# Kernel optimization log

Hardware: AMD Instinct MI355X
Metric: run time of the kernel (lower is better)

The kernel has to match this reference:

```python
import jax, jax.numpy as jnp
import numpy as np

# RT-DETR multi-scale deformable attention reference (PPMSDeformableAttention forward, value_mask=None)
SPATIAL_SHAPES = ((80, 80), (40, 40), (20, 20))  # (H, W) per level; sum(H*W) = 8400 = Len_v
NUM_HEADS = 8
NUM_LEVELS = 3
NUM_POINTS = 4


def _gather_corner(v_l, ix, iy, H, W):
    # v_l: [bs, heads, H*W, hd]; ix/iy: [bs, heads, N] int32 pixel indices (possibly out of range)
    valid = (ix >= 0) & (ix < W) & (iy >= 0) & (iy < H)
    idx = jnp.clip(iy, 0, H - 1) * W + jnp.clip(ix, 0, W - 1)
    g = jnp.take_along_axis(v_l, idx[..., None], axis=2)  # [bs, heads, N, hd]
    return jnp.where(valid[..., None], g, jnp.zeros((), v_l.dtype))


def _bilinear_sample(v_l, px, py, H, W):
    # grid_sample(align_corners=False, padding_mode='zeros') semantics.
    # v_l: [bs, heads, H*W, hd]; px/py: [bs, heads, N] continuous pixel coords
    x0 = jnp.floor(px).astype(jnp.int32)
    y0 = jnp.floor(py).astype(jnp.int32)
    x1, y1 = x0 + 1, y0 + 1
    wx1 = px - x0.astype(px.dtype)
    wy1 = py - y0.astype(py.dtype)
    wx0, wy0 = 1.0 - wx1, 1.0 - wy1
    out = (_gather_corner(v_l, x0, y0, H, W) * (wx0 * wy0)[..., None]
           + _gather_corner(v_l, x1, y0, H, W) * (wx1 * wy0)[..., None]
           + _gather_corner(v_l, x0, y1, H, W) * (wx0 * wy1)[..., None]
           + _gather_corner(v_l, x1, y1, H, W) * (wx1 * wy1)[..., None])
    return out  # [bs, heads, N, hd]


def setup_inputs() -> dict:
    key = jax.random.key(0)
    ks = jax.random.split(key, 8)
    bs, Lq, C = 32, 300, 256
    Lv = sum(h * w for h, w in SPATIAL_SHAPES)
    tp = NUM_HEADS * NUM_LEVELS * NUM_POINTS  # 96
    s = 1.0 / np.sqrt(C)
    return {
        "query": jax.random.normal(ks[0], (bs, Lq, C), jnp.float32),
        "reference_points": jax.random.uniform(ks[1], (bs, Lq, NUM_LEVELS, 4), jnp.float32, 0.05, 0.95),
        "value": jax.random.normal(ks[2], (bs, Lv, C), jnp.float32),
        "Wv": jax.random.normal(ks[3], (C, C), jnp.float32) * s,
        "bv": jnp.zeros((C,), jnp.float32),
        "Woff": jax.random.normal(ks[4], (C, tp * 2), jnp.float32) * (s * 0.1),
        "boff": jax.random.normal(ks[5], (tp * 2,), jnp.float32) * 0.5,
        "Watt": jax.random.normal(ks[6], (C, tp), jnp.float32) * s,
        "batt": jnp.zeros((tp,), jnp.float32),
        "Wout": jax.random.normal(ks[7], (C, C), jnp.float32) * s,
        "bout": jnp.zeros((C,), jnp.float32),
    }


def reference(query, reference_points, value, Wv, bv, Woff, boff, Watt, batt, Wout, bout):
    bs, Lq, C = query.shape
    H_, L, P = NUM_HEADS, NUM_LEVELS, NUM_POINTS
    hd = C // H_
    Lv = value.shape[1]

    # value projection -> [bs, heads, Lv, hd]
    v = (value @ Wv + bv).reshape(bs, Lv, H_, hd).transpose(0, 2, 1, 3)

    # sampling offsets and attention weights from query
    off = (query @ Woff + boff).reshape(bs, Lq, H_, L, P, 2)
    attw = jax.nn.softmax((query @ Watt + batt).reshape(bs, Lq, H_, L * P), axis=-1)
    attw = attw.reshape(bs, Lq, H_, L, P)

    # reference_points last dim == 4: (cx, cy, w, h) normalized
    ref_xy = reference_points[:, :, None, :, None, :2]  # [bs,Lq,1,L,1,2]
    ref_wh = reference_points[:, :, None, :, None, 2:]
    loc = ref_xy + off / P * ref_wh * 0.5  # [bs,Lq,H,L,P,2], normalized [0,1]

    out = jnp.zeros((bs, Lq, H_, hd), query.dtype)
    start = 0
    for l, (H, W) in enumerate(SPATIAL_SHAPES):
        v_l = v[:, :, start:start + H * W]  # [bs, heads, H*W, hd]
        start += H * W
        # normalized -> pixel coords (align_corners=False): p = loc * size - 0.5
        locl = loc[:, :, :, l]  # [bs, Lq, heads, P, 2]
        px = locl[..., 0] * W - 0.5
        py = locl[..., 1] * H - 0.5
        # [bs, Lq, heads, P] -> [bs, heads, Lq*P]
        px = px.transpose(0, 2, 1, 3).reshape(bs, H_, Lq * P)
        py = py.transpose(0, 2, 1, 3).reshape(bs, H_, Lq * P)
        sampled = _bilinear_sample(v_l, px, py, H, W)  # [bs, heads, Lq*P, hd]
        sampled = sampled.reshape(bs, H_, Lq, P, hd)
        out = out + jnp.einsum('bhqpd,bqhp->bqhd', sampled, attw[:, :, :, l])

    out = out.reshape(bs, Lq, C)
    return out @ Wout + bout
```

## Files before the change

kernel.cpp:

```cpp
#include <hip/hip_runtime.h>
#include <hip/hip_bf16.h>

#define BS 32
#define LQ 300
#define CDIM 256
#define HEADS 8
#define HD 32
#define NLEVELS 3
#define NPOINTS 4
#define LV 8400
#define NOA 288

typedef __attribute__((ext_vector_type(4))) float f32x4;
typedef __attribute__((ext_vector_type(8))) short short8;
typedef __attribute__((ext_vector_type(8))) unsigned short u16x8;
typedef __attribute__((ext_vector_type(4))) unsigned short u16x4;

__device__ __forceinline__ unsigned short f2bf(float f) {
    __hip_bfloat16 h = __float2bfloat16(f);
    return __bfloat16_as_ushort(h);
}
__device__ __forceinline__ float bf2f(unsigned short u) {
    union { unsigned u; float f; } v; v.u = ((unsigned)u) << 16;
    return v.f;
}

__global__ void prep_weights_kernel(
    const float* __restrict__ Wv, const float* __restrict__ Wout,
    const float* __restrict__ Woff, const float* __restrict__ Watt,
    unsigned short* __restrict__ WvT, unsigned short* __restrict__ WoutT,
    unsigned short* __restrict__ WoaT)
{
    const int bid = blockIdx.x;
    const int k = threadIdx.x;
    if (bid < 256) {
        WvT[bid * 256 + k] = f2bf(Wv[k * 256 + bid]);
    } else if (bid < 512) {
        const int n = bid - 256;
        WoutT[n * 256 + k] = f2bf(Wout[k * 256 + n]);
    } else {
        const int n = bid - 512;
        const float w = (n < 192) ? Woff[k * 192 + n] : Watt[k * 96 + (n - 192)];
        WoaT[n * 256 + k] = f2bf(w);
    }
}

#define BM 128
#define BMP 64
#define BK 32
#define PAD 40
#define EPAD 264
#define NT (CDIM / BK)

__global__ __launch_bounds__(256) void proj_value_mfma(
    const float* __restrict__ value, const unsigned short* __restrict__ WvT,
    const float* __restrict__ bv, unsigned short* __restrict__ vout)
{
    __shared__ alignas(16) unsigned short lds_w[2][256 * PAD];
    __shared__ alignas(16) unsigned short lds_x[2][BMP * PAD];
    unsigned short* lds_ep = &lds_w[0][0];

    const int tid = threadIdx.x;
    const int lane = tid & 63;
    const int wave = tid >> 6;
    const long row0 = (long)blockIdx.x * BMP;
    const int la = lane & 15;
    const int lg = lane >> 4;

    const unsigned short* wptr = WvT + (size_t)tid * CDIM;
    const int xr = tid >> 2, xk = (tid & 3) * 8;
    const float* xptr = value + (row0 + xr) * CDIM + xk;

    u16x8 wrg[4];
    f32x4 xrg[2];

    auto load_tile = [&](int kb) {
        const u16x8* qw = (const u16x8*)(wptr + kb);
        wrg[0] = qw[0]; wrg[1] = qw[1]; wrg[2] = qw[2]; wrg[3] = qw[3];
        const float* p = xptr + kb;
        xrg[0] = *(const f32x4*)(p);
        xrg[1] = *(const f32x4*)(p + 4);
    };
    auto write_tile = [&](int buf) {
        u16x8* ww = (u16x8*)&lds_w[buf][tid * PAD];
        ww[0] = wrg[0]; ww[1] = wrg[1]; ww[2] = wrg[2]; ww[3] = wrg[3];
        u16x8 t0;
#pragma unroll
        for (int i = 0; i < 4; ++i) {
            t0[i]     = f2bf(xrg[0][i]);
            t0[i + 4] = f2bf(xrg[1][i]);
        }
        *(u16x8*)&lds_x[buf][xr * PAD + xk] = t0;
    };

    f32x4 acc[4][4] = {};

    load_tile(0);
    write_tile(0);
    __syncthreads();
    int cur = 0;

    for (int t = 0; t < NT; ++t) {
        if (t + 1 < NT) load_tile((t + 1) * BK);

        const unsigned short* pw = &lds_w[cur][(wave * 64 + la) * PAD + lg * 8];
        const unsigned short* px = &lds_x[cur][la * PAD + lg * 8];
        short8 xf[4];
#pragma unroll
        for (int mf = 0; mf < 4; ++mf)
            xf[mf] = *(const short8*)(px + mf * 16 * PAD);
#pragma unroll
        for (int nf = 0; nf < 4; ++nf) {
            const short8 wf = *(const short8*)(pw + nf * 16 * PAD);
#pragma unroll
            for (int mf = 0; mf < 4; ++mf)
                acc[nf][mf] = __builtin_amdgcn_mfma_f32_16x16x32_bf16(wf, xf[mf], acc[nf][mf], 0, 0, 0);
        }

        if (t + 1 < NT) write_tile(cur ^ 1);
        __syncthreads();
        cur ^= 1;
    }

#pragma unroll
    for (int nf = 0; nf < 4; ++nf) {
        const int nbase = wave * 64 + nf * 16 + lg * 4;
        const f32x4 bb = *(const f32x4*)&bv[nbase];
#pragma unroll
        for (int mf = 0; mf < 4; ++mf) {
            const int mloc = mf * 16 + la;
            u16x4 o;
#pragma unroll
            for (int j = 0; j < 4; ++j) o[j] = f2bf(acc[nf][mf][j] + bb[j]);
            *(u16x4*)&lds_ep[mloc * EPAD + nbase] = o;
        }
    }
    __syncthreads();
    const int er = tid >> 2;
    const int ec = (tid & 3) * 64;
    const long gr = row0 + er;
    const u16x8* src = (const u16x8*)&lds_ep[er * EPAD + ec];
    u16x8* dst = (u16x8*)&vout[gr * CDIM + ec];
#pragma unroll
    for (int i = 0; i < 8; ++i) dst[i] = src[i];
}

#define APAD 40
#define BPAD 40

__global__ __launch_bounds__(256) void offatt_gemm_mfma(
    const float* __restrict__ query, const unsigned short* __restrict__ WoaT,
    const float* __restrict__ boff, const float* __restrict__ batt,
    float* __restrict__ offatt)
{
    __shared__ unsigned short lds_a[2][BM * APAD];
    __shared__ unsigned short lds_b[2][NOA * BPAD];

    const int tid = threadIdx.x;
    const int lane = tid & 63;
    const int wave = tid >> 6;
    const int wm = wave >> 1;
    const int wn = wave & 1;
    const long row0 = (long)blockIdx.x * BM;

    const int ar = tid >> 1;
    const int ak = (tid & 1) * 16;
    const float* aptr = query + (row0 + ar) * CDIM + ak;
    const unsigned short* bptr  = WoaT + (size_t)tid * CDIM;
    const unsigned short* bptr2 = WoaT + (size_t)(256 + tid) * CDIM;
    const bool extra = tid < 32;

    f32x4 arg[4];
    u16x8 brg[4], brg2[4];

    auto load_tile = [&](int kb) {
        const float* p = aptr + kb;
        arg[0] = *(const f32x4*)(p);
        arg[1] = *(const f32x4*)(p + 4);
        arg[2] = *(const f32x4*)(p + 8);
        arg[3] = *(const f32x4*)(p + 12);
        const u16x8* q = (const u16x8*)(bptr + kb);
        brg[0] = q[0]; brg[1] = q[1]; brg[2] = q[2]; brg[3] = q[3];
        if (extra) {
            const u16x8* q2 = (const u16x8*)(bptr2 + kb);
            brg2[0] = q2[0]; brg2[1] = q2[1]; brg2[2] = q2[2]; brg2[3] = q2[3];
        }
    };
    auto write_tile = [&](int buf) {
        u16x8 t0, t1;
#pragma unroll
        for (int i = 0; i < 4; ++i) {
            t0[i]     = f2bf(arg[0][i]);
            t0[i + 4] = f2bf(arg[1][i]);
            t1[i]     = f2bf(arg[2][i]);
            t1[i + 4] = f2bf(arg[3][i]);
        }
        u16x8* wa = (u16x8*)&lds_a[buf][ar * APAD + ak];
        wa[0] = t0; wa[1] = t1;
        u16x8* wb = (u16x8*)&lds_b[buf][tid * BPAD];
        wb[0] = brg[0]; wb[1] = brg[1]; wb[2] = brg[2]; wb[3] = brg[3];
        if (extra) {
            u16x8* wb2 = (u16x8*)&lds_b[buf][(256 + tid) * BPAD];
            wb2[0] = brg2[0]; wb2[1] = brg2[1]; wb2[2] = brg2[2]; wb2[3] = brg2[3];
        }
    };

    f32x4 acc[4][9] = {};
    const int la = lane & 15;
    const int lg = lane >> 4;

    load_tile(0);
    write_tile(0);
    __syncthreads();
    int cur = 0;

    for (int t = 0; t < CDIM / BK; ++t) {
        if (t + 1 < CDIM / BK) load_tile((t + 1) * BK);

        const unsigned short* pa = &lds_a[cur][(wm * 64 + la) * APAD + lg * 8];
        const unsigned short* pb = &lds_b[cur][(wn * 144 + la) * BPAD + lg * 8];
        short8 af[4];
#pragma unroll
        for (int mi = 0; mi < 4; ++mi)
            af[mi] = *(const short8*)(pa + mi * 16 * APAD);
#pragma unroll
        for (int ni = 0; ni < 9; ++ni) {
            const short8 bf = *(const short8*)(pb + ni * 16 * BPAD);
#pragma unroll
            for (int mi = 0; mi < 4; ++mi)
                acc[mi][ni] = __builtin_amdgcn_mfma_f32_16x16x32_bf16(af[mi], bf, acc[mi][ni], 0, 0, 0);
        }

        if (t + 1 < CDIM / BK) write_tile(cur ^ 1);
        __syncthreads();
        cur ^= 1;
    }

    float bias[9];
#pragma unroll
    for (int ni = 0; ni < 9; ++ni) {
        const int col = wn * 144 + ni * 16 + la;
        bias[ni] = (col < 192) ? boff[col] : batt[col - 192];
    }
#pragma unroll
    for (int mi = 0; mi < 4; ++mi) {
#pragma unroll
        for (int ni = 0; ni < 9; ++ni) {
            const int col = wn * 144 + ni * 16 + la;
#pragma unroll
            for (int j = 0; j < 4; ++j) {
                const long r = row0 + wm * 64 + mi * 16 + lg * 4 + j;
                offatt[r * NOA + col] = acc[mi][ni][j] + bias[ni];
            }
        }
    }
}

__global__ __launch_bounds__(256) void sample_kernel(
    const float* __restrict__ offatt, const float* __restrict__ refpts,
    const unsigned short* __restrict__ v, unsigned short* __restrict__ mid)
{
    __shared__ float oa_s[NOA];
    __shared__ float aw_s[96];
    __shared__ float px_s[96];
    __shared__ float py_s[96];

    const int tid = threadIdx.x;
    const int nb = blockIdx.x;
    const int x = nb & 7;
    const int rest = nb >> 3;
    const int g = rest / LQ;
    const int q = rest % LQ;
    const int b = g * 8 + x;
    const long bq = (long)b * LQ + q;

    oa_s[tid] = offatt[bq * NOA + tid];
    if (tid < 32) oa_s[256 + tid] = offatt[bq * NOA + 256 + tid];
    __syncthreads();

    if (tid < 8) {
        float m = -1e30f;
#pragma unroll
        for (int i = 0; i < 12; ++i) m = fmaxf(m, oa_s[192 + tid * 12 + i]);
        float e[12];
        float s = 0.f;
#pragma unroll
        for (int i = 0; i < 12; ++i) { e[i] = __expf(oa_s[192 + tid * 12 + i] - m); s += e[i]; }
        const float inv = 1.f / s;
#pragma unroll
        for (int i = 0; i < 12; ++i) aw_s[tid * 12 + i] = e[i] * inv;
    }
    if (tid >= 128 && tid < 224) {
        const int t = tid - 128;
        const int h = t / 12, idx = t % 12, l = idx >> 2, p = idx & 3;
        const float* rp = refpts + (bq * NLEVELS + l) * 4;
        const float rx = rp[0], ry = rp[1], rw = rp[2], rh = rp[3];
        const float ox = oa_s[((h * NLEVELS + l) * NPOINTS + p) * 2 + 0];
        const float oy = oa_s[((h * NLEVELS + l) * NPOINTS + p) * 2 + 1];
        const float lx = rx + ox * 0.125f * rw;
        const float ly = ry + oy * 0.125f * rh;
        const int Wl = 80 >> l;
        px_s[t] = lx * (float)Wl - 0.5f;
        py_s[t] = ly * (float)Wl - 0.5f;
    }
    __syncthreads();

    const int h = tid >> 5;
    const int pg = (tid >> 3) & 3;
    const int d4 = tid & 7;
    const unsigned short* vb = v + ((size_t)b * LV) * CDIM + h * HD + d4 * 4;

    float a0 = 0.f, a1 = 0.f, a2 = 0.f, a3 = 0.f;
#pragma unroll
    for (int j = 0; j < 3; ++j) {
        const int i = pg * 3 + j;
        const int l = i >> 2;
        const int idx = h * 12 + i;
        const float px = px_s[idx], py = py_s[idx], aw = aw_s[idx];
        const int Wl = 80 >> l;
        const int start = (l == 0) ? 0 : (l == 1) ? 6400 : 8000;

        const float fx = floorf(px), fy = floorf(py);
        const int x0 = (int)fx, y0 = (int)fy;
        const float wx1 = px - fx, wy1 = py - fy;
        const float wx0 = 1.f - wx1, wy0 = 1.f - wy1;
        const float w00 = wx0 * wy0 * aw, w10 = wx1 * wy0 * aw;
        const float w01 = wx0 * wy1 * aw, w11 = wx1 * wy1 * aw;
        const bool x0v = (unsigned)x0 < (unsigned)Wl;
        const bool x1v = (unsigned)(x0 + 1) < (unsigned)Wl;
        const bool y0v = (unsigned)y0 < (unsigned)Wl;
        const bool y1v = (unsigned)(y0 + 1) < (unsigned)Wl;

        const unsigned short* base = vb + (size_t)start * CDIM;
        if (y0v) {
            const unsigned short* r0p = base + (size_t)(y0 * Wl) * CDIM;
            if (x0v) {
                const u16x4 u = *(const u16x4*)(r0p + (size_t)x0 * CDIM);
                a0 = fmaf(w00, bf2f(u[0]), a0); a1 = fmaf(w00, bf2f(u[1]), a1);
                a2 = fmaf(w00, bf2f(u[2]), a2); a3 = fmaf(w00, bf2f(u[3]), a3);
            }
            if (x1v) {
                const u16x4 u = *(const u16x4*)(r0p + (size_t)(x0 + 1) * CDIM);
                a0 = fmaf(w10, bf2f(u[0]), a0); a1 = fmaf(w10, bf2f(u[1]), a1);
                a2 = fmaf(w10, bf2f(u[2]), a2); a3 = fmaf(w10, bf2f(u[3]), a3);
            }
        }
        if (y1v) {
            const unsigned short* r1p = base + (size_t)((y0 + 1) * Wl) * CDIM;
            if (x0v) {
                const u16x4 u = *(const u16x4*)(r1p + (size_t)x0 * CDIM);
                a0 = fmaf(w01, bf2f(u[0]), a0); a1 = fmaf(w01, bf2f(u[1]), a1);
                a2 = fmaf(w01, bf2f(u[2]), a2); a3 = fmaf(w01, bf2f(u[3]), a3);
            }
            if (x1v) {
                const u16x4 u = *(const u16x4*)(r1p + (size_t)(x0 + 1) * CDIM);
                a0 = fmaf(w11, bf2f(u[0]), a0); a1 = fmaf(w11, bf2f(u[1]), a1);
                a2 = fmaf(w11, bf2f(u[2]), a2); a3 = fmaf(w11, bf2f(u[3]), a3);
            }
        }
    }

    a0 += __shfl_xor(a0, 8);  a1 += __shfl_xor(a1, 8);
    a2 += __shfl_xor(a2, 8);  a3 += __shfl_xor(a3, 8);
    a0 += __shfl_xor(a0, 16); a1 += __shfl_xor(a1, 16);
    a2 += __shfl_xor(a2, 16); a3 += __shfl_xor(a3, 16);

    if (pg == 0) {
        u16x4 o;
        o[0] = f2bf(a0); o[1] = f2bf(a1); o[2] = f2bf(a2); o[3] = f2bf(a3);
        *(u16x4*)&mid[bq * CDIM + h * HD + d4 * 4] = o;
    }
}

__global__ __launch_bounds__(256) void out_gemm_mfma(
    const unsigned short* __restrict__ mid, const unsigned short* __restrict__ WoutT,
    const float* __restrict__ bout, float* __restrict__ out)
{
    __shared__ unsigned short lds_w[2][256 * APAD];
    __shared__ unsigned short lds_x[2][BM * BPAD];

    const int tid = threadIdx.x;
    const int lane = tid & 63;
    const int wave = tid >> 6;
    const int wn = wave & 1;
    const int wm = wave >> 1;
    const long row0 = (long)blockIdx.x * BM;

    const unsigned short* wptr = WoutT + (size_t)tid * CDIM;
    const int xr = tid >> 1;
    const int xk = (tid & 1) * 16;
    const unsigned short* xptr = mid + (row0 + xr) * CDIM + xk;

    u16x8 wrg[4];
    u16x8 xrg[2];

    auto load_tile = [&](int kb) {
        const u16x8* qw = (const u16x8*)(wptr + kb);
        wrg[0] = qw[0]; wrg[1] = qw[1]; wrg[2] = qw[2]; wrg[3] = qw[3];
        const u16x8* qx = (const u16x8*)(xptr + kb);
        xrg[0] = qx[0]; xrg[1] = qx[1];
    };
    auto write_tile = [&](int buf) {
        u16x8* ww = (u16x8*)&lds_w[buf][tid * APAD];
        ww[0] = wrg[0]; ww[1] = wrg[1]; ww[2] = wrg[2]; ww[3] = wrg[3];
        u16x8* wx = (u16x8*)&lds_x[buf][xr * BPAD + xk];
        wx[0] = xrg[0]; wx[1] = xrg[1];
    };

    f32x4 acc[8][4] = {};
    const int la = lane & 15;
    const int lg = lane >> 4;

    load_tile(0);
    write_tile(0);
    __syncthreads();
    int cur = 0;

    for (int t = 0; t < CDIM / BK; ++t) {
        if (t + 1 < CDIM / BK) load_tile((t + 1) * BK);

        const unsigned short* pw = &lds_w[cur][(wn * 128 + la) * APAD + lg * 8];
        const unsigned short* px = &lds_x[cur][(wm * 64 + la) * BPAD + lg * 8];
        short8 xf[4];
#pragma unroll
        for (int mf = 0; mf < 4; ++mf)
            xf[mf] = *(const short8*)(px + mf * 16 * BPAD);
#pragma unroll
        for (int nf = 0; nf < 8; ++nf) {
            const short8 wf = *(const short8*)(pw + nf * 16 * APAD);
#pragma unroll
            for (int mf = 0; mf < 4; ++mf)
                acc[nf][mf] = __builtin_amdgcn_mfma_f32_16x16x32_bf16(wf, xf[mf], acc[nf][mf], 0, 0, 0);
        }

        if (t + 1 < CDIM / BK) write_tile(cur ^ 1);
        __syncthreads();
        cur ^= 1;
    }

#pragma unroll
    for (int nf = 0; nf < 8; ++nf) {
        const int nbase = wn * 128 + nf * 16 + lg * 4;
        const f32x4 bb = *(const f32x4*)&bout[nbase];
#pragma unroll
        for (int mf = 0; mf < 4; ++mf) {
            const long m = row0 + wm * 64 + mf * 16 + la;
            f32x4 o;
#pragma unroll
            for (int j = 0; j < 4; ++j) o[j] = acc[nf][mf][j] + bb[j];
            *(f32x4*)&out[m * CDIM + nbase] = o;
        }
    }
}

extern "C" void kernel_launch(void* const* d_in, const int* in_sizes, int n_in,
                              void* d_out, int out_size, void* d_ws, size_t ws_size,
                              hipStream_t stream) {
    const float* query = (const float*)d_in[0];
    const float* refp  = (const float*)d_in[1];
    const float* value = (const float*)d_in[2];
    const float* Wv    = (const float*)d_in[3];
    const float* bv    = (const float*)d_in[4];
    const float* Woff  = (const float*)d_in[5];
    const float* boff  = (const float*)d_in[6];
    const float* Watt  = (const float*)d_in[7];
    const float* batt  = (const float*)d_in[8];
    const float* Wout  = (const float*)d_in[9];
    const float* bout  = (const float*)d_in[10];
    float* out = (float*)d_out;

    char* ws = (char*)d_ws;
    unsigned short* v = (unsigned short*)ws;
    size_t off = (size_t)BS * LV * CDIM * 2;
    float* offatt = (float*)(ws + off);
    off += (size_t)BS * LQ * NOA * 4;
    unsigned short* mid = (unsigned short*)(ws + off);
    off += (size_t)BS * LQ * CDIM * 2;
    unsigned short* WvT = (unsigned short*)(ws + off);
    off += 256 * 256 * 2;
    unsigned short* WoaT = (unsigned short*)(ws + off);
    off += NOA * 256 * 2;
    unsigned short* WoutT = (unsigned short*)(ws + off);

    prep_weights_kernel<<<800, 256, 0, stream>>>(Wv, Wout, Woff, Watt, WvT, WoutT, WoaT);
    proj_value_mfma<<<(BS * LV) / BMP, 256, 0, stream>>>(value, WvT, bv, v);
    offatt_gemm_mfma<<<(BS * LQ) / BM, 256, 0, stream>>>(query, WoaT, boff, batt, offatt);
    sample_kernel<<<BS * LQ, 256, 0, stream>>>(offatt, refp, v, mid);
    out_gemm_mfma<<<(BS * LQ) / BM, 256, 0, stream>>>(mid, WoutT, bout, out);
}
```

Before: 230.4 us.

## Retile value projection to 128x128 blocks with XCD-aware block remapping

The value projection GEMM moves from 64-row blocks that each cover all 256 output columns to 128x128 output tiles. Each wave now computes a 64x64 quadrant, and pairs of blocks share the same value rows. Block IDs are remapped so the two column halves of a row tile land on the same XCD, which lets them share L2 for the fp32 value reads. The goal is to cut per-block weight traffic and raise arithmetic intensity, at the cost of reading the fp32 activations twice across block pairs.

New measurement: 216.1 us. -6.2%, faster.

```diff
diff --git a/kernel.cpp b/kernel.cpp
--- a/kernel.cpp
+++ b/kernel.cpp
@@ -46,51 +46,64 @@
 }
 
 #define BM 128
-#define BMP 64
 #define BK 32
 #define PAD 40
-#define EPAD 264
+#define EP2 136
 #define NT (CDIM / BK)
 
 __global__ __launch_bounds__(256) void proj_value_mfma(
     const float* __restrict__ value, const unsigned short* __restrict__ WvT,
     const float* __restrict__ bv, unsigned short* __restrict__ vout)
 {
-    __shared__ alignas(16) unsigned short lds_w[2][256 * PAD];
-    __shared__ alignas(16) unsigned short lds_x[2][BMP * PAD];
-    unsigned short* lds_ep = &lds_w[0][0];
+    __shared__ alignas(16) unsigned short lds_raw[20480];
+    unsigned short* lds_w = lds_raw;
+    unsigned short* lds_x = lds_raw + 2 * 128 * PAD;
+    unsigned short* lds_ep = lds_raw;
 
     const int tid = threadIdx.x;
     const int lane = tid & 63;
     const int wave = tid >> 6;
-    const long row0 = (long)blockIdx.x * BMP;
+    const int wn = wave & 1;
+    const int wm = wave >> 1;
     const int la = lane & 15;
     const int lg = lane >> 4;
 
-    const unsigned short* wptr = WvT + (size_t)tid * CDIM;
-    const int xr = tid >> 2, xk = (tid & 3) * 8;
-    const float* xptr = value + (row0 + xr) * CDIM + xk;
-
-    u16x8 wrg[4];
-    f32x4 xrg[2];
+    const int orig = blockIdx.x;
+    const int xcd = orig & 7, lin = orig >> 3;
+    const int bid = xcd * 525 + lin;
+    const int n0 = (bid & 1) * 128;
+    const long row0 = (long)(bid >> 1) * BM;
+
+    const int sr = tid >> 1;
+    const int sk = (tid & 1) * 16;
+    const unsigned short* wptr = WvT + (size_t)(n0 + sr) * CDIM + sk;
+    const float* xptr = value + (row0 + sr) * (long)CDIM + sk;
+
+    u16x8 wrg[2];
+    f32x4 xrg[4];
 
     auto load_tile = [&](int kb) {
         const u16x8* qw = (const u16x8*)(wptr + kb);
-        wrg[0] = qw[0]; wrg[1] = qw[1]; wrg[2] = qw[2]; wrg[3] = qw[3];
+        wrg[0] = qw[0]; wrg[1] = qw[1];
         const float* p = xptr + kb;
         xrg[0] = *(const f32x4*)(p);
         xrg[1] = *(const f32x4*)(p + 4);
+        xrg[2] = *(const f32x4*)(p + 8);
+        xrg[3] = *(const f32x4*)(p + 12);
     };
     auto write_tile = [&](int buf) {
-        u16x8* ww = (u16x8*)&lds_w[buf][tid * PAD];
-        ww[0] = wrg[0]; ww[1] = wrg[1]; ww[2] = wrg[2]; ww[3] = wrg[3];
-        u16x8 t0;
+        u16x8* ww = (u16x8*)&lds_w[buf * (128 * PAD) + sr * PAD + sk];
+        ww[0] = wrg[0]; ww[1] = wrg[1];
+        u16x8 t0, t1;
 #pragma unroll
         for (int i = 0; i < 4; ++i) {
             t0[i]     = f2bf(xrg[0][i]);
             t0[i + 4] = f2bf(xrg[1][i]);
-        }
-        *(u16x8*)&lds_x[buf][xr * PAD + xk] = t0;
+            t1[i]     = f2bf(xrg[2][i]);
+            t1[i + 4] = f2bf(xrg[3][i]);
+        }
+        u16x8* wx = (u16x8*)&lds_x[buf * (128 * PAD) + sr * PAD + sk];
+        wx[0] = t0; wx[1] = t1;
     };
 
     f32x4 acc[4][4] = {};
@@ -103,8 +116,8 @@
     for (int t = 0; t < NT; ++t) {
         if (t + 1 < NT) load_tile((t + 1) * BK);
 
-        const unsigned short* pw = &lds_w[cur][(wave * 64 + la) * PAD + lg * 8];
-        const unsigned short* px = &lds_x[cur][la * PAD + lg * 8];
+        const unsigned short* pw = &lds_w[cur * (128 * PAD) + (wn * 64 + la) * PAD + lg * 8];
+        const unsigned short* px = &lds_x[cur * (128 * PAD) + (wm * 64 + la) * PAD + lg * 8];
         short8 xf[4];
 #pragma unroll
         for (int mf = 0; mf < 4; ++mf)
@@ -124,25 +137,26 @@
 
 #pragma unroll
     for (int nf = 0; nf < 4; ++nf) {
-        const int nbase = wave * 64 + nf * 16 + lg * 4;
-        const f32x4 bb = *(const f32x4*)&bv[nbase];
+        const int nbl = wn * 64 + nf * 16 + lg * 4;
+        const f32x4 bb = *(const f32x4*)&bv[n0 + nbl];
 #pragma unroll
         for (int mf = 0; mf < 4; ++mf) {
-            const int mloc = mf * 16 + la;
+            const int mloc = wm * 64 + mf * 16 + la;
             u16x4 o;
 #pragma unroll
             for (int j = 0; j < 4; ++j) o[j] = f2bf(acc[nf][mf][j] + bb[j]);
-            *(u16x4*)&lds_ep[mloc * EPAD + nbase] = o;
+            *(u16x4*)&lds_ep[mloc * EP2 + nbl] = o;
         }
     }
     __syncthreads();
-    const int er = tid >> 2;
-    const int ec = (tid & 3) * 64;
-    const long gr = row0 + er;
-    const u16x8* src = (const u16x8*)&lds_ep[er * EPAD + ec];
-    u16x8* dst = (u16x8*)&vout[gr * CDIM + ec];
-#pragma unroll
-    for (int i = 0; i < 8; ++i) dst[i] = src[i];
+    {
+        const int er = tid >> 1;
+        const int ec = (tid & 1) * 64;
+        const u16x8* src = (const u16x8*)&lds_ep[er * EP2 + ec];
+        u16x8* dst = (u16x8*)&vout[(row0 + er) * CDIM + n0 + ec];
+#pragma unroll
+        for (int i = 0; i < 8; ++i) dst[i] = src[i];
+    }
 }
 
 #define APAD 40
@@ -483,7 +497,7 @@
     unsigned short* WoutT = (unsigned short*)(ws + off);
 
     prep_weights_kernel<<<800, 256, 0, stream>>>(Wv, Wout, Woff, Watt, WvT, WoutT, WoaT);
-    proj_value_mfma<<<(BS * LV) / BMP, 256, 0, stream>>>(value, WvT, bv, v);
+    proj_value_mfma<<<(BS * LV) / BM * 2, 256, 0, stream>>>(value, WvT, bv, v);
     offatt_gemm_mfma<<<(BS * LQ) / BM, 256, 0, stream>>>(query, WoaT, boff, batt, offatt);
     sample_kernel<<<BS * LQ, 256, 0, stream>>>(offatt, refp, v, mid);
     out_gemm_mfma<<<(BS * LQ) / BM, 256, 0, stream>>>(mid, WoutT, bout, out);
```
